# Kernel tuning notes

Hardware: AMD Instinct MI355X
Metric: run time of the kernel (lower is better)

## Reference

```python
import jax, jax.numpy as jnp
import numpy as np

B, N, M, J, D, PF = 4, 131072, 10475, 55, 64, 486


def setup_inputs() -> dict:
    key = jax.random.key(0)
    ks = jax.random.split(key, 16)
    return {
        "pts": jax.random.normal(ks[0], (B, N, 3), jnp.float32),
        "betas": jax.random.normal(ks[1], (B, 10), jnp.float32),
        "pose_feature": jax.random.normal(ks[2], (B, PF), jnp.float32),
        "init_spdir": jax.random.normal(ks[3], (M, 3, 10), jnp.float32),
        "init_podir": jax.random.normal(ks[4], (PF, 3 * M), jnp.float32),
        "init_faces": jax.random.randint(ks[5], (N, 3), 0, M, jnp.int32),
        "tfs_A": jax.random.normal(ks[6], (B, J, 4, 4), jnp.float32),
        "tfs_inv": jax.random.normal(ks[7], (1, J, 4, 4), jnp.float32),
        "poseoff_cano": jax.random.normal(ks[8], (1, N, 3), jnp.float32),
        "lbsw": jax.random.uniform(ks[9], (1, N, J), jnp.float32),
        "lbs_voxel": jax.random.uniform(ks[10], (1, J, D, D, D), jnp.float32),
        "vox_scale": jnp.ones((1, 1, 3), jnp.float32),
        "vox_offset": jnp.zeros((1, 1, 3), jnp.float32),
        "mask": jax.random.randint(ks[11], (B, N), 0, 2, jnp.int32),
    }


def _trilinear(vox, x, scale, offset):
    # vox: [J,D,D,D], x: [b,n,3] -> [b,n,J] trilinearly interpolated weights
    nj, nd = vox.shape[0], vox.shape[-1]
    g = jnp.clip(x * scale + offset, -1.0, 1.0)          # normalized coords
    t = (g + 1.0) * 0.5 * (nd - 1)                        # voxel coords
    i0 = jnp.clip(jnp.floor(t), 0, nd - 2).astype(jnp.int32)
    f = t - i0                                            # fractional part
    vf = vox.reshape(nj, -1)                              # [J, D^3]
    out = jnp.zeros(x.shape[:-1] + (nj,), x.dtype)
    for dx in (0, 1):
        for dy in (0, 1):
            for dz in (0, 1):
                ix = i0[..., 0] + dx
                iy = i0[..., 1] + dy
                iz = i0[..., 2] + dz
                wgt = ((f[..., 0] if dx else 1.0 - f[..., 0]) *
                       (f[..., 1] if dy else 1.0 - f[..., 1]) *
                       (f[..., 2] if dz else 1.0 - f[..., 2]))
                fid = (ix * nd + iy) * nd + iz            # flat voxel index [b,n]
                out = out + wgt[..., None] * jnp.moveaxis(vf[:, fid], 0, -1)
    return out


def reference(pts, betas, pose_feature, init_spdir, init_podir, init_faces,
              tfs_A, tfs_inv, poseoff_cano, lbsw, lbs_voxel, vox_scale,
              vox_offset, mask):
    b, n, _ = pts.shape
    # blend-shape offsets on template vertices
    shape_full = jnp.einsum('bl,mkl->bmk', betas, init_spdir)      # [b,M,3]
    pose_full = (pose_feature @ init_podir).reshape(b, -1, 3)      # [b,M,3]
    # face-vertex gather then average over the 3 vertices of each face
    shape_off = shape_full[:, init_faces].mean(axis=2)             # [b,F,3]
    pose_off = pose_full[:, init_faces].mean(axis=2)               # [b,F,3]
    x = pts + shape_off + pose_off - poseoff_cano                  # canonical pts + offsets
    # voxel-grid skinning-weight lookup at canonical points
    w_vox = _trilinear(lbs_voxel[0], pts, vox_scale, vox_offset)   # [b,n,J]
    w = jnp.where(mask[..., None] > 0, lbsw, w_vox)
    w = w / jnp.clip(w.sum(-1, keepdims=True), 1e-8)
    # per-point blended transforms: A @ A_inv_template
    tfs = tfs_A @ tfs_inv                                          # [b,J,4,4]
    T = jnp.einsum('bnj,bjrc->bnrc', w, tfs)                       # [b,n,4,4]
    xh = jnp.concatenate([x, jnp.ones_like(x[..., :1])], axis=-1)
    posed = jnp.einsum('bnrc,bnc->bnr', T, xh)[..., :3]
    return posed.reshape(b, n, 1, 3), T
```

## Files before the change

### kernel.cpp

```cpp
#include <hip/hip_runtime.h>

#define B_  4
#define N_  131072
#define J_  55
#define JP_ 56
#define D_  64
#define D3_ 262144
#define PF_ 486
#define COLS_ 31425

#define BL16(u) __uint_as_float((u) << 16)
#define BH16(u) __uint_as_float((u) & 0xffff0000u)

typedef float vfloat4 __attribute__((ext_vector_type(4)));

__device__ __forceinline__ unsigned short f2bf(float v) {
    unsigned u = __float_as_uint(v);
    u += 0x7fffu + ((u >> 16) & 1u);
    return (unsigned short)(u >> 16);
}

__global__ void k_off_pose(const float* __restrict__ pf,
                           const float* __restrict__ podir,
                           const float* __restrict__ betas,
                           const float* __restrict__ spdir,
                           float* __restrict__ off_full) {
    int col = blockIdx.x * 256 + threadIdx.x;
    if (col >= COLS_) return;
    int pc = blockIdx.y;
    float a0 = 0.f, a1 = 0.f, a2 = 0.f, a3 = 0.f;
    if (pc == 0) {
        float sp[10];
#pragma unroll
        for (int l = 0; l < 10; ++l) sp[l] = spdir[col * 10 + l];
#pragma unroll
        for (int l = 0; l < 10; ++l) {
            a0 += betas[0 * 10 + l] * sp[l];
            a1 += betas[1 * 10 + l] * sp[l];
            a2 += betas[2 * 10 + l] * sp[l];
            a3 += betas[3 * 10 + l] * sp[l];
        }
    }
    int p0 = pc * 61;
    int p1 = p0 + 61; if (p1 > PF_) p1 = PF_;
    int p = p0;
    for (; p + 4 <= p1; p += 4) {
        float v0 = podir[(size_t)(p + 0) * COLS_ + col];
        float v1 = podir[(size_t)(p + 1) * COLS_ + col];
        float v2 = podir[(size_t)(p + 2) * COLS_ + col];
        float v3 = podir[(size_t)(p + 3) * COLS_ + col];
        a0 += pf[0 * PF_ + p] * v0 + pf[0 * PF_ + p + 1] * v1 +
              pf[0 * PF_ + p + 2] * v2 + pf[0 * PF_ + p + 3] * v3;
        a1 += pf[1 * PF_ + p] * v0 + pf[1 * PF_ + p + 1] * v1 +
              pf[1 * PF_ + p + 2] * v2 + pf[1 * PF_ + p + 3] * v3;
        a2 += pf[2 * PF_ + p] * v0 + pf[2 * PF_ + p + 1] * v1 +
              pf[2 * PF_ + p + 2] * v2 + pf[2 * PF_ + p + 3] * v3;
        a3 += pf[3 * PF_ + p] * v0 + pf[3 * PF_ + p + 1] * v1 +
              pf[3 * PF_ + p + 2] * v2 + pf[3 * PF_ + p + 3] * v3;
    }
    for (; p < p1; ++p) {
        float v = podir[(size_t)p * COLS_ + col];
        a0 += pf[0 * PF_ + p] * v;
        a1 += pf[1 * PF_ + p] * v;
        a2 += pf[2 * PF_ + p] * v;
        a3 += pf[3 * PF_ + p] * v;
    }
    atomicAdd(&off_full[0 * COLS_ + col], a0);
    atomicAdd(&off_full[1 * COLS_ + col], a1);
    atomicAdd(&off_full[2 * COLS_ + col], a2);
    atomicAdd(&off_full[3 * COLS_ + col], a3);
}

__global__ void k_tfs(const float* __restrict__ A,
                      const float* __restrict__ Ainv,
                      float* __restrict__ tfsP) {
    int tid = blockIdx.x * 256 + threadIdx.x;
    if (tid >= B_ * JP_ * 16) return;
    int rc = tid & 15;
    int jb = tid >> 4;
    int j = jb % JP_;
    int b = jb / JP_;
    float v = 0.f;
    if (j < J_) {
        int r = rc >> 2, c = rc & 3;
#pragma unroll
        for (int k = 0; k < 4; ++k)
            v += A[((b * J_ + j) * 4 + r) * 4 + k] * Ainv[(j * 4 + k) * 4 + c];
    }
    tfsP[tid] = v;
}

__global__ __launch_bounds__(256) void k_G(
    const float* __restrict__ vox, const float* __restrict__ tfsP,
    uint4* __restrict__ Gtb, float* __restrict__ Stb) {
    int v = blockIdx.x * 256 + threadIdx.x;
    float g[4][16];
    float s = 0.f;
#pragma unroll
    for (int b = 0; b < 4; ++b)
#pragma unroll
        for (int r = 0; r < 16; ++r) g[b][r] = 0.f;
    for (int j0 = 0; j0 < J_; j0 += 5) {
        float wv[5];
#pragma unroll
        for (int k = 0; k < 5; ++k)
            wv[k] = vox[(size_t)(j0 + k) * D3_ + v];
#pragma unroll
        for (int k = 0; k < 5; ++k) {
            float w = wv[k];
            s += w;
#pragma unroll
            for (int b = 0; b < 4; ++b) {
                const float* tr = tfsP + (b * JP_ + j0 + k) * 16;
#pragma unroll
                for (int r = 0; r < 16; ++r) g[b][r] += w * tr[r];
            }
        }
    }
    Stb[v] = s;
#pragma unroll
    for (int b = 0; b < 4; ++b) {
        unsigned gw[8];
#pragma unroll
        for (int k = 0; k < 8; ++k)
            gw[k] = (unsigned)f2bf(g[b][2 * k]) |
                    ((unsigned)f2bf(g[b][2 * k + 1]) << 16);
        uint4* gp = Gtb + ((size_t)b * D3_ + v) * 2;
        gp[0] = make_uint4(gw[0], gw[1], gw[2], gw[3]);
        gp[1] = make_uint4(gw[4], gw[5], gw[6], gw[7]);
    }
}

#define ACC8(Toff, qa, qb)                                 \
    T[Toff + 0] += w0 * BL16(qa.x) + w1 * BL16(qb.x);      \
    T[Toff + 1] += w0 * BH16(qa.x) + w1 * BH16(qb.x);      \
    T[Toff + 2] += w0 * BL16(qa.y) + w1 * BL16(qb.y);      \
    T[Toff + 3] += w0 * BH16(qa.y) + w1 * BH16(qb.y);      \
    T[Toff + 4] += w0 * BL16(qa.z) + w1 * BL16(qb.z);      \
    T[Toff + 5] += w0 * BH16(qa.z) + w1 * BH16(qb.z);      \
    T[Toff + 6] += w0 * BL16(qa.w) + w1 * BL16(qb.w);      \
    T[Toff + 7] += w0 * BH16(qa.w) + w1 * BH16(qb.w);

__global__ __launch_bounds__(256) void k_main(
    const float* __restrict__ pts, const int* __restrict__ faces,
    const float* __restrict__ poseoff, const int* __restrict__ mask,
    const float* __restrict__ vox_scale, const float* __restrict__ vox_offset,
    const float* __restrict__ off_full, const float* __restrict__ tfsP,
    const float* __restrict__ lbsw, const uint4* __restrict__ Gtb,
    const float* __restrict__ Stb,
    float* __restrict__ out_posed, float* __restrict__ out_T) {
    __shared__ float sx0[256], sx1[256], sx2[256];
    __shared__ float sf0[256], sf1[256], sf2[256];
    __shared__ int   scell[256];
    __shared__ unsigned short lst[256];
    __shared__ int wc[4];

    int bid = blockIdx.x;
    int b  = (bid >> 1) & 3;
    int nc = ((bid >> 3) << 1) | (bid & 1);
    int tid = threadIdx.x;
    int n = nc * 256 + tid;
    int i = (b << 17) | n;

    float px = pts[3 * i + 0], py = pts[3 * i + 1], pz = pts[3 * i + 2];
    int f0 = faces[3 * n + 0], f1 = faces[3 * n + 1], f2 = faces[3 * n + 2];
    const float* ob = off_full + b * COLS_;
    const float c3 = 1.f / 3.f;
    float ox = (ob[f0 * 3 + 0] + ob[f1 * 3 + 0] + ob[f2 * 3 + 0]) * c3;
    float oy = (ob[f0 * 3 + 1] + ob[f1 * 3 + 1] + ob[f2 * 3 + 1]) * c3;
    float oz = (ob[f0 * 3 + 2] + ob[f1 * 3 + 2] + ob[f2 * 3 + 2]) * c3;
    sx0[tid] = px + ox - poseoff[3 * n + 0];
    sx1[tid] = py + oy - poseoff[3 * n + 1];
    sx2[tid] = pz + oz - poseoff[3 * n + 2];

    bool isv = !(mask[i] > 0);
    if (isv) {
        float sxc = vox_scale[0], syc = vox_scale[1], szc = vox_scale[2];
        float o0 = vox_offset[0], o1 = vox_offset[1], o2 = vox_offset[2];
        float gx = fminf(fmaxf(px * sxc + o0, -1.f), 1.f);
        float gy = fminf(fmaxf(py * syc + o1, -1.f), 1.f);
        float gz = fminf(fmaxf(pz * szc + o2, -1.f), 1.f);
        float tx = (gx + 1.f) * 0.5f * (D_ - 1);
        float ty = (gy + 1.f) * 0.5f * (D_ - 1);
        float tz = (gz + 1.f) * 0.5f * (D_ - 1);
        int ix = (int)floorf(tx); if (ix > D_ - 2) ix = D_ - 2; if (ix < 0) ix = 0;
        int iy = (int)floorf(ty); if (iy > D_ - 2) iy = D_ - 2; if (iy < 0) iy = 0;
        int iz = (int)floorf(tz); if (iz > D_ - 2) iz = D_ - 2; if (iz < 0) iz = 0;
        sf0[tid] = tx - ix;
        sf1[tid] = ty - iy;
        sf2[tid] = tz - iz;
        scell[tid] = (ix * D_ + iy) * D_ + iz;
    }

    unsigned long long bal = __ballot(isv);
    int lane = tid & 63, wid = tid >> 6;
    if (lane == 0) wc[wid] = __popcll(bal);
    __syncthreads();
    int pre = 0;
#pragma unroll
    for (int k = 0; k < 4; ++k) pre += (k < wid) ? wc[k] : 0;
    int tot = wc[0] + wc[1] + wc[2] + wc[3];
    unsigned long long lt = ((unsigned long long)1 << lane) - 1ull;
    int vbefore = pre + __popcll(bal & lt);
    int pos = isv ? vbefore : (tot + (tid - vbefore));
    lst[pos] = (unsigned short)tid;
    __syncthreads();

    int slot = lst[tid];
    float x0 = sx0[slot], x1 = sx1[slot], x2 = sx2[slot];
    int ii = (b << 17) | (nc * 256 + slot);

    float T[16];
#pragma unroll
    for (int r = 0; r < 16; ++r) T[r] = 0.f;
    float wsum = 0.f;

    if (tid < tot) {
        float fx = sf0[slot], fy = sf1[slot], fz = sf2[slot];
        int cell = scell[slot];
        const uint4* Gb = Gtb + (size_t)b * D3_ * 2;
#pragma unroll
        for (int cc = 0; cc < 4; ++cc) {
            int fid = cell + ((cc & 2) ? D_ * D_ : 0) + ((cc & 1) ? D_ : 0);
            float wxy = ((cc & 2) ? fx : 1.f - fx) * ((cc & 1) ? fy : 1.f - fy);
            float w0 = wxy * (1.f - fz);
            float w1 = wxy * fz;
            const uint4* R = Gb + (size_t)fid * 2;
            uint4 q0 = R[0], q1 = R[1], q2 = R[2], q3 = R[3];
            wsum += w0 * Stb[fid] + w1 * Stb[fid + 1];
            ACC8(0, q0, q2)
            ACC8(8, q1, q3)
        }
    } else {
        int n2 = nc * 256 + slot;
        const float* lw = lbsw + (size_t)n2 * J_;
        const float* tb = tfsP + b * (JP_ * 16);
        float wv[8];
        for (int c = 0; c < 6; ++c) {
#pragma unroll
            for (int k = 0; k < 8; ++k) wv[k] = lw[c * 8 + k];
#pragma unroll
            for (int k = 0; k < 8; ++k) {
                float w = wv[k];
                wsum += w;
                const float* tr = tb + (c * 8 + k) * 16;
#pragma unroll
                for (int r = 0; r < 16; ++r) T[r] += w * tr[r];
            }
        }
#pragma unroll
        for (int k = 0; k < 7; ++k) wv[k] = lw[48 + k];
#pragma unroll
        for (int k = 0; k < 7; ++k) {
            float w = wv[k];
            wsum += w;
            const float* tr = tb + (48 + k) * 16;
#pragma unroll
            for (int r = 0; r < 16; ++r) T[r] += w * tr[r];
        }
    }

    float inv = 1.f / fmaxf(wsum, 1e-8f);
    float t[16];
#pragma unroll
    for (int r = 0; r < 16; ++r) t[r] = T[r] * inv;
    out_posed[3 * ii + 0] = t[0] * x0 + t[1] * x1 + t[2] * x2 + t[3];
    out_posed[3 * ii + 1] = t[4] * x0 + t[5] * x1 + t[6] * x2 + t[7];
    out_posed[3 * ii + 2] = t[8] * x0 + t[9] * x1 + t[10] * x2 + t[11];
    vfloat4* to = (vfloat4*)(out_T + (size_t)ii * 16);
    vfloat4 r0 = { t[0], t[1], t[2], t[3] };
    vfloat4 r1 = { t[4], t[5], t[6], t[7] };
    vfloat4 r2 = { t[8], t[9], t[10], t[11] };
    vfloat4 r3 = { t[12], t[13], t[14], t[15] };
    __builtin_nontemporal_store(r0, to + 0);
    __builtin_nontemporal_store(r1, to + 1);
    __builtin_nontemporal_store(r2, to + 2);
    __builtin_nontemporal_store(r3, to + 3);
}

extern "C" void kernel_launch(void* const* d_in, const int* in_sizes, int n_in,
                              void* d_out, int out_size, void* d_ws, size_t ws_size,
                              hipStream_t stream) {
    const float* pts      = (const float*)d_in[0];
    const float* betas    = (const float*)d_in[1];
    const float* pf       = (const float*)d_in[2];
    const float* spdir    = (const float*)d_in[3];
    const float* podir    = (const float*)d_in[4];
    const int*   faces    = (const int*)d_in[5];
    const float* tfs_A    = (const float*)d_in[6];
    const float* tfs_inv  = (const float*)d_in[7];
    const float* poseoff  = (const float*)d_in[8];
    const float* lbsw     = (const float*)d_in[9];
    const float* vox      = (const float*)d_in[10];
    const float* vscale   = (const float*)d_in[11];
    const float* voffset  = (const float*)d_in[12];
    const int*   mask     = (const int*)d_in[13];

    char* w = (char*)d_ws;
    uint4* Gtb      = (uint4*)w;
    float* Stb      = (float*)(w + 33554432);
    float* off_full = (float*)(w + 34603008);
    float* tfsP     = (float*)(w + 35106048);

    float* out_posed = (float*)d_out;
    float* out_T     = out_posed + (size_t)B_ * N_ * 3;

    (void)hipMemsetAsync(off_full, 0, 503040, stream);
    k_tfs<<<(B_ * JP_ * 16 + 255) / 256, 256, 0, stream>>>(tfs_A, tfs_inv, tfsP);
    k_G<<<D3_ / 256, 256, 0, stream>>>(vox, tfsP, Gtb, Stb);
    dim3 gpose((COLS_ + 255) / 256, 8);
    k_off_pose<<<gpose, 256, 0, stream>>>(pf, podir, betas, spdir, off_full);

    k_main<<<2048, 256, 0, stream>>>(pts, faces, poseoff, mask, vscale, voffset,
                                     off_full, tfsP, lbsw, Gtb, Stb,
                                     out_posed, out_T);
}
```

Measured before the change: 293.5 us.

## Fuse voxel transform precompute and blend-shape offsets into one prelude kernel

Merges the voxel-grid transform precompute and the pose/shape offset GEMV into a single launch whose blocks are split by index. The offset part no longer splits PF across blocks, so the memset and atomics go away at the cost of fewer, longer blocks. It also loads all 55 voxel weights up front, vectorises the lbsw row loads in the masked path, and switches the T output from nontemporal to normal stores. The fully unrolled 55-value preload raises register pressure and could lower occupancy in the prelude.

New measurement: 359.5 us. +22.5%, slower.

```diff
diff --git a/kernel.cpp b/kernel.cpp
--- a/kernel.cpp
+++ b/kernel.cpp
@@ -9,10 +9,13 @@
 #define PF_ 486
 #define COLS_ 31425
 
+#define GZ_ 1024
+#define OZ_ 123
+
 #define BL16(u) __uint_as_float((u) << 16)
 #define BH16(u) __uint_as_float((u) & 0xffff0000u)
 
-typedef float vfloat4 __attribute__((ext_vector_type(4)));
+typedef float f4a __attribute__((ext_vector_type(4), aligned(4)));
 
 __device__ __forceinline__ unsigned short f2bf(float v) {
     unsigned u = __float_as_uint(v);
@@ -20,60 +23,9 @@
     return (unsigned short)(u >> 16);
 }
 
-__global__ void k_off_pose(const float* __restrict__ pf,
-                           const float* __restrict__ podir,
-                           const float* __restrict__ betas,
-                           const float* __restrict__ spdir,
-                           float* __restrict__ off_full) {
-    int col = blockIdx.x * 256 + threadIdx.x;
-    if (col >= COLS_) return;
-    int pc = blockIdx.y;
-    float a0 = 0.f, a1 = 0.f, a2 = 0.f, a3 = 0.f;
-    if (pc == 0) {
-        float sp[10];
-#pragma unroll
-        for (int l = 0; l < 10; ++l) sp[l] = spdir[col * 10 + l];
-#pragma unroll
-        for (int l = 0; l < 10; ++l) {
-            a0 += betas[0 * 10 + l] * sp[l];
-            a1 += betas[1 * 10 + l] * sp[l];
-            a2 += betas[2 * 10 + l] * sp[l];
-            a3 += betas[3 * 10 + l] * sp[l];
-        }
-    }
-    int p0 = pc * 61;
-    int p1 = p0 + 61; if (p1 > PF_) p1 = PF_;
-    int p = p0;
-    for (; p + 4 <= p1; p += 4) {
-        float v0 = podir[(size_t)(p + 0) * COLS_ + col];
-        float v1 = podir[(size_t)(p + 1) * COLS_ + col];
-        float v2 = podir[(size_t)(p + 2) * COLS_ + col];
-        float v3 = podir[(size_t)(p + 3) * COLS_ + col];
-        a0 += pf[0 * PF_ + p] * v0 + pf[0 * PF_ + p + 1] * v1 +
-              pf[0 * PF_ + p + 2] * v2 + pf[0 * PF_ + p + 3] * v3;
-        a1 += pf[1 * PF_ + p] * v0 + pf[1 * PF_ + p + 1] * v1 +
-              pf[1 * PF_ + p + 2] * v2 + pf[1 * PF_ + p + 3] * v3;
-        a2 += pf[2 * PF_ + p] * v0 + pf[2 * PF_ + p + 1] * v1 +
-              pf[2 * PF_ + p + 2] * v2 + pf[2 * PF_ + p + 3] * v3;
-        a3 += pf[3 * PF_ + p] * v0 + pf[3 * PF_ + p + 1] * v1 +
-              pf[3 * PF_ + p + 2] * v2 + pf[3 * PF_ + p + 3] * v3;
-    }
-    for (; p < p1; ++p) {
-        float v = podir[(size_t)p * COLS_ + col];
-        a0 += pf[0 * PF_ + p] * v;
-        a1 += pf[1 * PF_ + p] * v;
-        a2 += pf[2 * PF_ + p] * v;
-        a3 += pf[3 * PF_ + p] * v;
-    }
-    atomicAdd(&off_full[0 * COLS_ + col], a0);
-    atomicAdd(&off_full[1 * COLS_ + col], a1);
-    atomicAdd(&off_full[2 * COLS_ + col], a2);
-    atomicAdd(&off_full[3 * COLS_ + col], a3);
-}
-
-__global__ void k_tfs(const float* __restrict__ A,
-                      const float* __restrict__ Ainv,
-                      float* __restrict__ tfsP) {
+__global__ __launch_bounds__(256) void k_tfs(const float* __restrict__ A,
+                                             const float* __restrict__ Ainv,
+                                             float* __restrict__ tfsP) {
     int tid = blockIdx.x * 256 + threadIdx.x;
     if (tid >= B_ * JP_ * 16) return;
     int rc = tid & 15;
@@ -90,44 +42,90 @@
     tfsP[tid] = v;
 }
 
-__global__ __launch_bounds__(256) void k_G(
+__global__ __launch_bounds__(256) void k_prelude(
     const float* __restrict__ vox, const float* __restrict__ tfsP,
-    uint4* __restrict__ Gtb, float* __restrict__ Stb) {
-    int v = blockIdx.x * 256 + threadIdx.x;
-    float g[4][16];
-    float s = 0.f;
-#pragma unroll
-    for (int b = 0; b < 4; ++b)
-#pragma unroll
-        for (int r = 0; r < 16; ++r) g[b][r] = 0.f;
-    for (int j0 = 0; j0 < J_; j0 += 5) {
-        float wv[5];
-#pragma unroll
-        for (int k = 0; k < 5; ++k)
-            wv[k] = vox[(size_t)(j0 + k) * D3_ + v];
-#pragma unroll
-        for (int k = 0; k < 5; ++k) {
-            float w = wv[k];
+    uint4* __restrict__ Gtb, float* __restrict__ Stb,
+    const float* __restrict__ pf, const float* __restrict__ podir,
+    const float* __restrict__ betas, const float* __restrict__ spdir,
+    float* __restrict__ off_full) {
+    int bx = blockIdx.x;
+    int tid = threadIdx.x;
+
+    if (bx < GZ_) {
+        int v = bx * 256 + tid;
+        float wv[J_];
+#pragma unroll
+        for (int j = 0; j < J_; ++j) wv[j] = vox[(size_t)j * D3_ + v];
+        float g[4][16];
+        float s = 0.f;
+#pragma unroll
+        for (int b = 0; b < 4; ++b)
+#pragma unroll
+            for (int r = 0; r < 16; ++r) g[b][r] = 0.f;
+#pragma unroll
+        for (int j = 0; j < J_; ++j) {
+            float w = wv[j];
             s += w;
 #pragma unroll
             for (int b = 0; b < 4; ++b) {
-                const float* tr = tfsP + (b * JP_ + j0 + k) * 16;
+                const float* tr = tfsP + (b * JP_ + j) * 16;
 #pragma unroll
                 for (int r = 0; r < 16; ++r) g[b][r] += w * tr[r];
             }
         }
-    }
-    Stb[v] = s;
-#pragma unroll
-    for (int b = 0; b < 4; ++b) {
-        unsigned gw[8];
-#pragma unroll
-        for (int k = 0; k < 8; ++k)
-            gw[k] = (unsigned)f2bf(g[b][2 * k]) |
-                    ((unsigned)f2bf(g[b][2 * k + 1]) << 16);
-        uint4* gp = Gtb + ((size_t)b * D3_ + v) * 2;
-        gp[0] = make_uint4(gw[0], gw[1], gw[2], gw[3]);
-        gp[1] = make_uint4(gw[4], gw[5], gw[6], gw[7]);
+        Stb[v] = s;
+#pragma unroll
+        for (int b = 0; b < 4; ++b) {
+            unsigned gw[8];
+#pragma unroll
+            for (int k = 0; k < 8; ++k)
+                gw[k] = (unsigned)f2bf(g[b][2 * k]) |
+                        ((unsigned)f2bf(g[b][2 * k + 1]) << 16);
+            uint4* gp = Gtb + ((size_t)b * D3_ + v) * 2;
+            gp[0] = make_uint4(gw[0], gw[1], gw[2], gw[3]);
+            gp[1] = make_uint4(gw[4], gw[5], gw[6], gw[7]);
+        }
+    } else {
+        int col = (bx - GZ_) * 256 + tid;
+        if (col >= COLS_) return;
+        float a0 = 0.f, a1 = 0.f, a2 = 0.f, a3 = 0.f;
+        {
+            float sp[10];
+#pragma unroll
+            for (int l = 0; l < 10; ++l) sp[l] = spdir[col * 10 + l];
+#pragma unroll
+            for (int l = 0; l < 10; ++l) {
+                a0 += betas[0 * 10 + l] * sp[l];
+                a1 += betas[1 * 10 + l] * sp[l];
+                a2 += betas[2 * 10 + l] * sp[l];
+                a3 += betas[3 * 10 + l] * sp[l];
+            }
+        }
+        int p = 0;
+        for (; p + 16 <= PF_; p += 16) {
+            float v16[16];
+#pragma unroll
+            for (int k = 0; k < 16; ++k)
+                v16[k] = podir[(size_t)(p + k) * COLS_ + col];
+#pragma unroll
+            for (int k = 0; k < 16; ++k) {
+                a0 += pf[0 * PF_ + p + k] * v16[k];
+                a1 += pf[1 * PF_ + p + k] * v16[k];
+                a2 += pf[2 * PF_ + p + k] * v16[k];
+                a3 += pf[3 * PF_ + p + k] * v16[k];
+            }
+        }
+        for (; p < PF_; ++p) {
+            float v = podir[(size_t)p * COLS_ + col];
+            a0 += pf[0 * PF_ + p] * v;
+            a1 += pf[1 * PF_ + p] * v;
+            a2 += pf[2 * PF_ + p] * v;
+            a3 += pf[3 * PF_ + p] * v;
+        }
+        off_full[0 * COLS_ + col] = a0;
+        off_full[1 * COLS_ + col] = a1;
+        off_full[2 * COLS_ + col] = a2;
+        off_full[3 * COLS_ + col] = a3;
     }
 }
 
@@ -156,7 +154,7 @@
     __shared__ int wc[4];
 
     int bid = blockIdx.x;
-    int b  = (bid >> 1) & 3;
+    int b  = (bid & 7) >> 1;
     int nc = ((bid >> 3) << 1) | (bid & 1);
     int tid = threadIdx.x;
     int n = nc * 256 + tid;
@@ -234,27 +232,29 @@
     } else {
         int n2 = nc * 256 + slot;
         const float* lw = lbsw + (size_t)n2 * J_;
+        f4a q[13];
+#pragma unroll
+        for (int k = 0; k < 13; ++k)
+            q[k] = *(const f4a*)(lw + 4 * k);
+        float w52 = lw[52], w53 = lw[53], w54 = lw[54];
         const float* tb = tfsP + b * (JP_ * 16);
-        float wv[8];
-        for (int c = 0; c < 6; ++c) {
-#pragma unroll
-            for (int k = 0; k < 8; ++k) wv[k] = lw[c * 8 + k];
-#pragma unroll
-            for (int k = 0; k < 8; ++k) {
-                float w = wv[k];
+#pragma unroll
+        for (int k = 0; k < 13; ++k) {
+#pragma unroll
+            for (int m = 0; m < 4; ++m) {
+                float w = q[k][m];
                 wsum += w;
-                const float* tr = tb + (c * 8 + k) * 16;
+                const float* tr = tb + (k * 4 + m) * 16;
 #pragma unroll
                 for (int r = 0; r < 16; ++r) T[r] += w * tr[r];
             }
         }
-#pragma unroll
-        for (int k = 0; k < 7; ++k) wv[k] = lw[48 + k];
-#pragma unroll
-        for (int k = 0; k < 7; ++k) {
-            float w = wv[k];
+        float wt[3] = { w52, w53, w54 };
+#pragma unroll
+        for (int m = 0; m < 3; ++m) {
+            float w = wt[m];
             wsum += w;
-            const float* tr = tb + (48 + k) * 16;
+            const float* tr = tb + (52 + m) * 16;
 #pragma unroll
             for (int r = 0; r < 16; ++r) T[r] += w * tr[r];
         }
@@ -267,15 +267,11 @@
     out_posed[3 * ii + 0] = t[0] * x0 + t[1] * x1 + t[2] * x2 + t[3];
     out_posed[3 * ii + 1] = t[4] * x0 + t[5] * x1 + t[6] * x2 + t[7];
     out_posed[3 * ii + 2] = t[8] * x0 + t[9] * x1 + t[10] * x2 + t[11];
-    vfloat4* to = (vfloat4*)(out_T + (size_t)ii * 16);
-    vfloat4 r0 = { t[0], t[1], t[2], t[3] };
-    vfloat4 r1 = { t[4], t[5], t[6], t[7] };
-    vfloat4 r2 = { t[8], t[9], t[10], t[11] };
-    vfloat4 r3 = { t[12], t[13], t[14], t[15] };
-    __builtin_nontemporal_store(r0, to + 0);
-    __builtin_nontemporal_store(r1, to + 1);
-    __builtin_nontemporal_store(r2, to + 2);
-    __builtin_nontemporal_store(r3, to + 3);
+    float4* to = (float4*)(out_T + (size_t)ii * 16);
+    to[0] = make_float4(t[0], t[1], t[2], t[3]);
+    to[1] = make_float4(t[4], t[5], t[6], t[7]);
+    to[2] = make_float4(t[8], t[9], t[10], t[11]);
+    to[3] = make_float4(t[12], t[13], t[14], t[15]);
 }
 
 extern "C" void kernel_launch(void* const* d_in, const int* in_sizes, int n_in,
@@ -300,18 +296,15 @@
     uint4* Gtb      = (uint4*)w;
     float* Stb      = (float*)(w + 33554432);
     float* off_full = (float*)(w + 34603008);
-    float* tfsP     = (float*)(w + 35106048);
+    float* tfsP     = (float*)(w + 35119104);
 
     float* out_posed = (float*)d_out;
     float* out_T     = out_posed + (size_t)B_ * N_ * 3;
 
-    (void)hipMemsetAsync(off_full, 0, 503040, stream);
-    k_tfs<<<(B_ * JP_ * 16 + 255) / 256, 256, 0, stream>>>(tfs_A, tfs_inv, tfsP);
-    k_G<<<D3_ / 256, 256, 0, stream>>>(vox, tfsP, Gtb, Stb);
-    dim3 gpose((COLS_ + 255) / 256, 8);
-    k_off_pose<<<gpose, 256, 0, stream>>>(pf, podir, betas, spdir, off_full);
-
-    k_main<<<2048, 256, 0, stream>>>(pts, faces, poseoff, mask, vscale, voffset,
-                                     off_full, tfsP, lbsw, Gtb, Stb,
+    k_tfs<<<14, 256, 0, stream>>>(tfs_A, tfs_inv, tfsP);
+    k_prelude<<<GZ_ + OZ_, 256, 0, stream>>>(
+        vox, tfsP, Gtb, Stb, pf, podir, betas, spdir, off_full);
+    k_main<<<2048, 256, 0, stream>>>(pts, faces, poseoff, mask, vscale,
+                                     voffset, off_full, tfsP, lbsw, Gtb, Stb,
                                      out_posed, out_T);
 }
```
